# Optimization experiments

Measured on AMD Instinct MI355X. Metric: run time of the kernel, lower is better.

Reference implementation:

```python
import jax, jax.numpy as jnp
import numpy as np

N_NODES = 89250


def _sage_conv(x, src, dst, w_l, w_r, b):
    # mean aggregation of neighbor messages x[src] at destination nodes
    msg = x[src]                                                # [E, C]
    agg = jax.ops.segment_sum(msg, dst, num_segments=N_NODES)   # [N, C]
    cnt = jax.ops.segment_sum(jnp.ones((src.shape[0],), x.dtype), dst,
                              num_segments=N_NODES)             # [N]
    mean = agg / jnp.clip(cnt, 1.0, None)[:, None]
    # PyG SAGEConv: lin_l(aggregated) + lin_r(x) + bias
    return mean @ w_l.T + x @ w_r.T + b


def setup_inputs() -> dict:
    key = jax.random.key(0)
    ks = jax.random.split(key, 9)
    N, E, F_IN = N_NODES, 899756, 500

    def glorot(k, shape):
        fan_in = shape[1]
        return jax.random.normal(k, shape, jnp.float32) / jnp.sqrt(jnp.float32(fan_in))

    x = jax.random.normal(ks[0], (N, F_IN), jnp.float32)
    edge_index = jax.random.randint(ks[1], (2, E), 0, N, jnp.int64 if jax.config.jax_enable_x64 else jnp.int32)
    return {
        "x": x,
        "edge_index": edge_index,
        "w_l1": glorot(ks[2], (512, F_IN)),
        "w_r1": glorot(ks[3], (512, F_IN)),
        "b1": jnp.zeros((512,), jnp.float32),
        "w_l2": glorot(ks[4], (256, 512)),
        "w_r2": glorot(ks[5], (256, 512)),
        "b2": jnp.zeros((256,), jnp.float32),
        "w_l3": glorot(ks[6], (7, 256)),
        "w_r3": glorot(ks[7], (7, 256)),
        "b3": jnp.zeros((7,), jnp.float32),
    }


def reference(x, edge_index, w_l1, w_r1, b1, w_l2, w_r2, b2, w_l3, w_r3, b3):
    src, dst = edge_index[0], edge_index[1]
    # eval mode: dropout is identity
    h = jax.nn.relu(_sage_conv(x, src, dst, w_l1, w_r1, b1))
    h = jax.nn.relu(_sage_conv(h, src, dst, w_l2, w_r2, b2))
    return _sage_conv(h, src, dst, w_l3, w_r3, b3)
```

## Files before the change

### kernel.cpp

```cpp
#include <hip/hip_runtime.h>
#include <cstdint>
#include <cstddef>

#define N_NODES 89250
#define M_PAD   89344
#define F0 500
#define F1 512
#define F2 256
#define F3 7
#define KP 512

typedef __attribute__((ext_vector_type(8))) short bf16x8;
typedef __attribute__((ext_vector_type(4))) float f32x4;

static inline int cdiv_i(int a, int b) { return (a + b - 1) / b; }

__device__ __forceinline__ unsigned short f2b(float f) {
  unsigned int u = __float_as_uint(f);
  u = (u + 0x7FFFu + ((u >> 16) & 1u)) >> 16;
  return (unsigned short)u;
}
__device__ __forceinline__ float b2f(unsigned short h) {
  return __uint_as_float(((unsigned int)h) << 16);
}

__global__ void degree_kernel(const int* __restrict__ dst, int* __restrict__ cnt, int E) {
  int stride = gridDim.x * blockDim.x;
  for (int i = blockIdx.x * blockDim.x + threadIdx.x; i < E; i += stride)
    atomicAdd(&cnt[dst[i]], 1);
}

__global__ __launch_bounds__(1024) void scan_partial(const int* __restrict__ cnt,
                                                     int* __restrict__ row_ptr,
                                                     int* __restrict__ bsum, int n) {
  __shared__ int sm[1024];
  const int i = blockIdx.x * 1024 + threadIdx.x;
  const int v = (i < n) ? cnt[i] : 0;
  sm[threadIdx.x] = v;
  __syncthreads();
  for (int off = 1; off < 1024; off <<= 1) {
    int t = (threadIdx.x >= off) ? sm[threadIdx.x - off] : 0;
    __syncthreads();
    sm[threadIdx.x] += t;
    __syncthreads();
  }
  if (i < n) row_ptr[i] = sm[threadIdx.x] - v;
  if (threadIdx.x == 1023) bsum[blockIdx.x] = sm[1023];
}

__global__ __launch_bounds__(1024) void scan_bsums(int* __restrict__ bsum, int nb) {
  __shared__ int sm[1024];
  const int v = (threadIdx.x < nb) ? bsum[threadIdx.x] : 0;
  sm[threadIdx.x] = v;
  __syncthreads();
  for (int off = 1; off < 1024; off <<= 1) {
    int t = (threadIdx.x >= off) ? sm[threadIdx.x - off] : 0;
    __syncthreads();
    sm[threadIdx.x] += t;
    __syncthreads();
  }
  if (threadIdx.x < nb) bsum[threadIdx.x] = sm[threadIdx.x] - v;
}

__global__ __launch_bounds__(1024) void scan_add(int* __restrict__ row_ptr,
                                                 const int* __restrict__ bsum,
                                                 int* __restrict__ cursor,
                                                 int n, int total) {
  const int i = blockIdx.x * 1024 + threadIdx.x;
  if (i < n) {
    const int v = row_ptr[i] + bsum[i >> 10];
    row_ptr[i] = v;
    cursor[i] = v;
  }
  if (i == 0) row_ptr[n] = total;
}

__global__ void fill_kernel(const int* __restrict__ src, const int* __restrict__ dst,
                            int* __restrict__ cursor, int* __restrict__ csr_src, int E) {
  int stride = gridDim.x * blockDim.x;
  for (int i = blockIdx.x * blockDim.x + threadIdx.x; i < E; i += stride) {
    const int p = atomicAdd(&cursor[dst[i]], 1);
    csr_src[p] = src[i];
  }
}

#define XBLK (M_PAD * 64 / 256)
__global__ __launch_bounds__(256) void prep_kernel(
    const float* __restrict__ x,
    const float* __restrict__ wl1, const float* __restrict__ wr1,
    const float* __restrict__ wl2, const float* __restrict__ wr2,
    const float* __restrict__ wl3, const float* __restrict__ wr3,
    unsigned short* __restrict__ xb,
    unsigned short* __restrict__ wl1b, unsigned short* __restrict__ wr1b,
    unsigned short* __restrict__ w2b, unsigned short* __restrict__ w3b)
{
  if (blockIdx.x < XBLK) {
    const int idx = blockIdx.x * 256 + threadIdx.x;
    const int node = idx >> 6;
    const int c8 = (idx & 63) * 8;
    unsigned short r[8];
#pragma unroll
    for (int j = 0; j < 8; ++j) {
      const int c = c8 + j;
      float v = 0.0f;
      if (node < N_NODES && c < F0) v = x[(size_t)node * F0 + c];
      r[j] = f2b(v);
    }
    *reinterpret_cast<uint4*>(xb + (size_t)node * KP + c8) = *reinterpret_cast<const uint4*>(r);
    return;
  }
  int idx = (blockIdx.x - XBLK) * 256 + threadIdx.x;
  const int S1 = F1 * KP;
  if (idx < S1) {
    const int j = idx >> 9, k = idx & 511;
    const bool in = (k < F0);
    wl1b[idx] = in ? f2b(wl1[(size_t)j * F0 + k]) : (unsigned short)0;
    wr1b[idx] = in ? f2b(wr1[(size_t)j * F0 + k]) : (unsigned short)0;
    return;
  }
  idx -= S1;
  const int S2 = F2 * KP;
  if (idx < S2) {
    w2b[idx] = f2b(wl2[idx]);
    w2b[S2 + idx] = f2b(wr2[idx]);
    return;
  }
  idx -= S2;
  if (idx < 16 * 256) {
    const int j = idx >> 8, k = idx & 255;
    float v = 0.0f;
    if (j < 7) v = wl3[(size_t)j * F2 + k];
    else if (j >= 8 && j < 15) v = wr3[(size_t)(j - 8) * F2 + k];
    w3b[idx] = f2b(v);
  }
}

__global__ __launch_bounds__(256) void gather_mean_bf512(
    const unsigned short* __restrict__ xb, const int* __restrict__ row_ptr,
    const int* __restrict__ csr_src, unsigned short* __restrict__ aggb)
{
  const int node = blockIdx.x * 4 + (threadIdx.x >> 6);
  const int t = threadIdx.x & 63;
  if (node >= M_PAD) return;
  if (node >= N_NODES) {
    *reinterpret_cast<uint4*>(aggb + (size_t)node * 512 + t * 8) = make_uint4(0, 0, 0, 0);
    return;
  }
  const int beg = row_ptr[node];
  const int end = row_ptr[node + 1];
  float acc[8] = {0.f, 0.f, 0.f, 0.f, 0.f, 0.f, 0.f, 0.f};
  for (int j = beg; j < end; j += 8) {
    uint4 v[8];
    float m[8];
#pragma unroll
    for (int u = 0; u < 8; ++u) {
      const int e = min(j + u, end - 1);
      m[u] = (j + u < end) ? 1.0f : 0.0f;
      v[u] = *reinterpret_cast<const uint4*>(xb + (size_t)csr_src[e] * 512 + t * 8);
    }
#pragma unroll
    for (int u = 0; u < 8; ++u) {
      const unsigned int w[4] = {v[u].x, v[u].y, v[u].z, v[u].w};
#pragma unroll
      for (int q = 0; q < 4; ++q) {
        acc[2 * q]     = fmaf(m[u], b2f((unsigned short)(w[q] & 0xFFFF)), acc[2 * q]);
        acc[2 * q + 1] = fmaf(m[u], b2f((unsigned short)(w[q] >> 16)),    acc[2 * q + 1]);
      }
    }
  }
  const int deg = end - beg;
  const float inv = 1.0f / (float)(deg > 1 ? deg : 1);
  unsigned short r[8];
#pragma unroll
  for (int q = 0; q < 8; ++q) r[q] = f2b(acc[q] * inv);
  *reinterpret_cast<uint4*>(aggb + (size_t)node * 512 + t * 8) = *reinterpret_cast<const uint4*>(r);
}

__global__ __launch_bounds__(256) void gemm_mfma(
    const unsigned short* __restrict__ A1, const unsigned short* __restrict__ A2,
    const unsigned short* __restrict__ B1, const unsigned short* __restrict__ B2,
    const float* __restrict__ bias, unsigned short* __restrict__ Cout,
    int J, int niter, int fuse, int relu)
{
  __shared__ __align__(16) unsigned short Alds[128 * 64];
  __shared__ __align__(16) unsigned short Blds[128 * 64];
  const int tid = threadIdx.x;
  const int lane = tid & 63;
  const int wid = tid >> 6;

  const int nwg = gridDim.x * gridDim.y;
  int wg = blockIdx.y * gridDim.x + blockIdx.x;
  const int cpx = nwg >> 3;
  wg = (wg & 7) * cpx + (wg >> 3);
  const int brow = (wg / gridDim.y) * 128;
  const int bcol = (wg % gridDim.y) * 128;

  const int wr = wid >> 1;
  const int wc = wid & 1;

  f32x4 acc[4][4];
#pragma unroll
  for (int m = 0; m < 4; ++m)
#pragma unroll
    for (int n = 0; n < 4; ++n) acc[m][n] = (f32x4){0.f, 0.f, 0.f, 0.f};

  const int srow = lane >> 3;
  const int schunk = (lane & 7) ^ srow;
  const int fr = lane & 15;
  const int fk = lane >> 4;

  for (int it = 0; it < niter; ++it) {
    const unsigned short* __restrict__ A = (it < 8) ? A1 : A2;
    const unsigned short* __restrict__ B = (it < 8) ? B1 : B2;
    const int k0 = (it & 7) * 64;
    __syncthreads();
#pragma unroll
    for (int i = 0; i < 4; ++i) {
      const int rbase = i * 32 + wid * 8;
      const int row = rbase + srow;
      __builtin_amdgcn_global_load_lds(
          (const __attribute__((address_space(1))) unsigned int*)(A + (size_t)(brow + row) * KP + k0 + schunk * 8),
          (__attribute__((address_space(3))) unsigned int*)(&Alds[rbase * 64]),
          16, 0, 0);
      __builtin_amdgcn_global_load_lds(
          (const __attribute__((address_space(1))) unsigned int*)(B + (size_t)(bcol + row) * KP + k0 + schunk * 8),
          (__attribute__((address_space(3))) unsigned int*)(&Blds[rbase * 64]),
          16, 0, 0);
    }
    __syncthreads();
#pragma unroll
    for (int ks = 0; ks < 2; ++ks) {
      bf16x8 a[4], b[4];
#pragma unroll
      for (int m = 0; m < 4; ++m) {
        const int row = wr * 64 + m * 16 + fr;
        a[m] = *reinterpret_cast<const bf16x8*>(&Alds[row * 64 + (((ks * 4 + fk) ^ (row & 7)) * 8)]);
      }
#pragma unroll
      for (int n = 0; n < 4; ++n) {
        const int row = wc * 64 + n * 16 + fr;
        b[n] = *reinterpret_cast<const bf16x8*>(&Blds[row * 64 + (((ks * 4 + fk) ^ (row & 7)) * 8)]);
      }
#pragma unroll
      for (int m = 0; m < 4; ++m)
#pragma unroll
        for (int n = 0; n < 4; ++n)
          acc[m][n] = __builtin_amdgcn_mfma_f32_16x16x32_bf16(a[m], b[n], acc[m][n], 0, 0, 0);
    }
  }

  const int crow0 = brow + wr * 64 + (lane >> 4) * 4;
  const int ccol0 = bcol + wc * 64 + (lane & 15);
#pragma unroll
  for (int n = 0; n < 4; ++n) {
    const int col = ccol0 + n * 16;
    const float bv = fuse ? bias[col] : 0.0f;
#pragma unroll
    for (int m = 0; m < 4; ++m) {
#pragma unroll
      for (int i = 0; i < 4; ++i) {
        const int row = crow0 + m * 16 + i;
        float v = acc[m][n][i] + bv;
        if (relu) v = fmaxf(v, 0.0f);
        Cout[(size_t)row * J + col] = f2b(v);
      }
    }
  }
}

__global__ __launch_bounds__(256) void combine2p3_kernel(
    const unsigned short* __restrict__ y, const int* __restrict__ row_ptr,
    const int* __restrict__ csr_src, const float* __restrict__ bias,
    const unsigned short* __restrict__ w3b, unsigned short* __restrict__ y3)
{
  __shared__ unsigned short w3s[16 * 256];
  {
    const int t0 = threadIdx.x * 16;
    *reinterpret_cast<uint4*>(&w3s[t0])     = *reinterpret_cast<const uint4*>(&w3b[t0]);
    *reinterpret_cast<uint4*>(&w3s[t0 + 8]) = *reinterpret_cast<const uint4*>(&w3b[t0 + 8]);
  }
  __syncthreads();

  const int node = blockIdx.x * 8 + (threadIdx.x >> 5);
  const int t = threadIdx.x & 31;
  if (node >= N_NODES) return;
  const int beg = row_ptr[node];
  const int end = row_ptr[node + 1];
  float acc[8] = {0.f, 0.f, 0.f, 0.f, 0.f, 0.f, 0.f, 0.f};
  for (int j = beg; j < end; j += 8) {
    uint4 v[8];
    float m[8];
#pragma unroll
    for (int u = 0; u < 8; ++u) {
      const int e = min(j + u, end - 1);
      m[u] = (j + u < end) ? 1.0f : 0.0f;
      v[u] = *reinterpret_cast<const uint4*>(y + (size_t)csr_src[e] * 512 + t * 8);
    }
#pragma unroll
    for (int u = 0; u < 8; ++u) {
      const unsigned int w[4] = {v[u].x, v[u].y, v[u].z, v[u].w};
#pragma unroll
      for (int q = 0; q < 4; ++q) {
        acc[2 * q]     = fmaf(m[u], b2f((unsigned short)(w[q] & 0xFFFF)), acc[2 * q]);
        acc[2 * q + 1] = fmaf(m[u], b2f((unsigned short)(w[q] >> 16)),    acc[2 * q + 1]);
      }
    }
  }
  const int deg = end - beg;
  const float inv = 1.0f / (float)(deg > 1 ? deg : 1);
  const uint4 rv = *reinterpret_cast<const uint4*>(y + (size_t)node * 512 + 256 + t * 8);
  const unsigned int ru[4] = {rv.x, rv.y, rv.z, rv.w};
  float c[8];
#pragma unroll
  for (int q = 0; q < 4; ++q) {
    const float y0 = b2f((unsigned short)(ru[q] & 0xFFFF));
    const float y1 = b2f((unsigned short)(ru[q] >> 16));
    c[2 * q]     = fmaxf(acc[2 * q] * inv + y0 + bias[t * 8 + 2 * q], 0.0f);
    c[2 * q + 1] = fmaxf(acc[2 * q + 1] * inv + y1 + bias[t * 8 + 2 * q + 1], 0.0f);
  }
#pragma unroll
  for (int jj = 0; jj < 14; ++jj) {
    const int row = jj + (jj >= 7 ? 1 : 0);
    const uint4 wv = *reinterpret_cast<const uint4*>(&w3s[row * 256 + t * 8]);
    const unsigned int wu[4] = {wv.x, wv.y, wv.z, wv.w};
    float s = 0.0f;
#pragma unroll
    for (int q = 0; q < 4; ++q) {
      s = fmaf(c[2 * q],     b2f((unsigned short)(wu[q] & 0xFFFF)), s);
      s = fmaf(c[2 * q + 1], b2f((unsigned short)(wu[q] >> 16)),    s);
    }
#pragma unroll
    for (int m = 1; m < 32; m <<= 1) s += __shfl_xor(s, m, 64);
    if (t == 0) y3[(size_t)node * 16 + row] = f2b(s);
  }
}

__global__ __launch_bounds__(256) void combine3_kernel(
    const unsigned short* __restrict__ y3, const int* __restrict__ row_ptr,
    const int* __restrict__ csr_src, const float* __restrict__ b3,
    float* __restrict__ out, int N)
{
  const int node = blockIdx.x * 4 + (threadIdx.x >> 6);
  const int lane = threadIdx.x & 63;
  if (node >= N) return;
  const int beg = row_ptr[node];
  const int end = row_ptr[node + 1];
  float acc[7] = {0.f, 0.f, 0.f, 0.f, 0.f, 0.f, 0.f};
  for (int j = beg + lane; j < end; j += 64) {
    const int s = csr_src[j];
    const uint4 v = *reinterpret_cast<const uint4*>(y3 + (size_t)s * 16);
    const unsigned int u[4] = {v.x, v.y, v.z, v.w};
#pragma unroll
    for (int q = 0; q < 7; ++q) {
      const unsigned short hw = (unsigned short)((u[q >> 1] >> ((q & 1) * 16)) & 0xFFFF);
      acc[q] += b2f(hw);
    }
  }
#pragma unroll
  for (int q = 0; q < 7; ++q)
#pragma unroll
    for (int m = 1; m < 64; m <<= 1)
      acc[q] += __shfl_xor(acc[q], m, 64);
  if (lane == 0) {
    const int deg = end - beg;
    const float inv = 1.0f / (float)(deg > 1 ? deg : 1);
    const uint4 rv = *reinterpret_cast<const uint4*>(y3 + (size_t)node * 16 + 8);
    const unsigned int ru[4] = {rv.x, rv.y, rv.z, rv.w};
#pragma unroll
    for (int q = 0; q < 7; ++q) {
      const float self = b2f((unsigned short)((ru[q >> 1] >> ((q & 1) * 16)) & 0xFFFF));
      out[(size_t)node * F3 + q] = acc[q] * inv + self + b3[q];
    }
  }
}

extern "C" void kernel_launch(void* const* d_in, const int* in_sizes, int n_in,
                              void* d_out, int out_size, void* d_ws, size_t ws_size,
                              hipStream_t stream) {
  const float* x    = (const float*)d_in[0];
  const int*   ei   = (const int*)d_in[1];
  const float* w_l1 = (const float*)d_in[2];
  const float* w_r1 = (const float*)d_in[3];
  const float* b1   = (const float*)d_in[4];
  const float* w_l2 = (const float*)d_in[5];
  const float* w_r2 = (const float*)d_in[6];
  const float* b2   = (const float*)d_in[7];
  const float* w_l3 = (const float*)d_in[8];
  const float* w_r3 = (const float*)d_in[9];
  const float* b3   = (const float*)d_in[10];
  float* out = (float*)d_out;

  const int E = in_sizes[1] / 2;
  const int* src = ei;
  const int* dst = ei + E;

  char* p = (char*)d_ws;
  int* row_ptr = (int*)p;           p += (size_t)(N_NODES + 1) * 4;
  int* cnt     = (int*)p;           p += (size_t)N_NODES * 4;
  int* bsum    = (int*)p;           p += 1024 * 4;
  int* csr_src = (int*)p;           p += (size_t)E * 4;
  p = (char*)(((uintptr_t)p + 255) & ~(uintptr_t)255);
  unsigned short* xb   = (unsigned short*)p;  p += (size_t)M_PAD * KP * 2;
  unsigned short* aggb = (unsigned short*)p;  p += (size_t)M_PAD * KP * 2;
  unsigned short* h1b  = (unsigned short*)p;  p += (size_t)M_PAD * KP * 2;
  unsigned short* wl1b = (unsigned short*)p;  p += (size_t)F1 * KP * 2;
  unsigned short* wr1b = (unsigned short*)p;  p += (size_t)F1 * KP * 2;
  unsigned short* w2b  = (unsigned short*)p;  p += (size_t)F1 * KP * 2;
  unsigned short* w3b  = (unsigned short*)p;  p += (size_t)16 * F2 * 2;

  unsigned short* y2  = xb;
  unsigned short* y3  = h1b;

  const int nb = cdiv_i(N_NODES, 1024);

  hipMemsetAsync(cnt, 0, (size_t)N_NODES * sizeof(int), stream);
  degree_kernel<<<cdiv_i(E, 256), 256, 0, stream>>>(dst, cnt, E);
  scan_partial<<<nb, 1024, 0, stream>>>(cnt, row_ptr, bsum, N_NODES);
  scan_bsums<<<1, 1024, 0, stream>>>(bsum, nb);
  scan_add<<<nb, 1024, 0, stream>>>(row_ptr, bsum, cnt, N_NODES, E);
  fill_kernel<<<cdiv_i(E, 256), 256, 0, stream>>>(src, dst, cnt, csr_src, E);

  {
    const int wblocks = cdiv_i(F1 * KP + F2 * KP + 16 * F2, 256);
    prep_kernel<<<XBLK + wblocks, 256, 0, stream>>>(
        x, w_l1, w_r1, w_l2, w_r2, w_l3, w_r3, xb, wl1b, wr1b, w2b, w3b);
  }

  gather_mean_bf512<<<cdiv_i(M_PAD, 4), 256, 0, stream>>>(xb, row_ptr, csr_src, aggb);
  {
    dim3 g(M_PAD / 128, F1 / 128);
    gemm_mfma<<<g, 256, 0, stream>>>(aggb, xb, wl1b, wr1b, b1, h1b, F1, 16, 1, 1);
  }

  {
    dim3 g(M_PAD / 128, 512 / 128);
    gemm_mfma<<<g, 256, 0, stream>>>(h1b, h1b, w2b, w2b, (const float*)nullptr, y2, 512, 8, 0, 0);
  }
  combine2p3_kernel<<<cdiv_i(N_NODES, 8), 256, 0, stream>>>(y2, row_ptr, csr_src, b2, w3b, y3);

  combine3_kernel<<<cdiv_i(N_NODES, 4), 256, 0, stream>>>(y3, row_ptr, csr_src, b3, out, N_NODES);
}
```

Before: 637.5 us.

## Use 256x256 double-buffered MFMA GEMM tiles with 8 waves and prefetch

The bf16 MFMA GEMM moves from 128x128 tiles with 4 waves to 256x256 tiles with 8 waves per block. The LDS buffers for A and B are now double-buffered so the next K-slice loads overlap the current MFMA work, with one barrier per iteration instead of two. Wave priority is raised around the MFMA bursts and the XCD block remapping now handles grid sizes that do not divide by 8. The larger tiles raise operand reuse and cut global traffic, but use 128KB of LDS and more accumulator registers, which limits occupancy to about one block per CU and leaves fewer blocks in the grid.

```diff
diff --git a/kernel.cpp b/kernel.cpp
--- a/kernel.cpp
+++ b/kernel.cpp
@@ -176,87 +176,106 @@
   *reinterpret_cast<uint4*>(aggb + (size_t)node * 512 + t * 8) = *reinterpret_cast<const uint4*>(r);
 }
 
-__global__ __launch_bounds__(256) void gemm_mfma(
+__global__ __launch_bounds__(512) void gemm_mfma256(
     const unsigned short* __restrict__ A1, const unsigned short* __restrict__ A2,
     const unsigned short* __restrict__ B1, const unsigned short* __restrict__ B2,
     const float* __restrict__ bias, unsigned short* __restrict__ Cout,
-    int J, int niter, int fuse, int relu)
+    int J, int nt, int fuse, int relu)
 {
-  __shared__ __align__(16) unsigned short Alds[128 * 64];
-  __shared__ __align__(16) unsigned short Blds[128 * 64];
+  __shared__ __align__(16) unsigned short Alds[2][256 * 64];
+  __shared__ __align__(16) unsigned short Blds[2][256 * 64];
   const int tid = threadIdx.x;
   const int lane = tid & 63;
-  const int wid = tid >> 6;
-
-  const int nwg = gridDim.x * gridDim.y;
-  int wg = blockIdx.y * gridDim.x + blockIdx.x;
-  const int cpx = nwg >> 3;
-  wg = (wg & 7) * cpx + (wg >> 3);
-  const int brow = (wg / gridDim.y) * 128;
-  const int bcol = (wg % gridDim.y) * 128;
-
-  const int wr = wid >> 1;
-  const int wc = wid & 1;
-
-  f32x4 acc[4][4];
-#pragma unroll
-  for (int m = 0; m < 4; ++m)
+  const int w = tid >> 6;
+  const int wm = w >> 2;
+  const int wn = w & 3;
+
+  int wg = blockIdx.x;
+  {
+    const int nwg = gridDim.x;
+    const int q = nwg >> 3, r = nwg & 7;
+    const int xcd = wg & 7, o = wg >> 3;
+    wg = (xcd < r ? xcd * (q + 1) : r * (q + 1) + (xcd - r) * q) + o;
+  }
+  const int ncol = J >> 8;
+  const int brow = (wg / ncol) * 256;
+  const int bcol = (wg % ncol) * 256;
+
+  f32x4 acc[8][4];
+#pragma unroll
+  for (int m = 0; m < 8; ++m)
 #pragma unroll
     for (int n = 0; n < 4; ++n) acc[m][n] = (f32x4){0.f, 0.f, 0.f, 0.f};
 
+  const int fr = lane & 15;
+  const int fk = lane >> 4;
   const int srow = lane >> 3;
   const int schunk = (lane & 7) ^ srow;
-  const int fr = lane & 15;
-  const int fk = lane >> 4;
-
-  for (int it = 0; it < niter; ++it) {
-    const unsigned short* __restrict__ A = (it < 8) ? A1 : A2;
-    const unsigned short* __restrict__ B = (it < 8) ? B1 : B2;
-    const int k0 = (it & 7) * 64;
-    __syncthreads();
-#pragma unroll
-    for (int i = 0; i < 4; ++i) {
-      const int rbase = i * 32 + wid * 8;
+
+  auto STAGE_H = [&](int t, int which) {
+    const int h = which >> 1;
+    const int k0 = (t & 7) * 64;
+    const int buf = t & 1;
+    const unsigned short* __restrict__ src;
+    unsigned short* ldsb;
+    if (which & 1) { src = (t < 8) ? B1 : B2; ldsb = Blds[buf]; }
+    else           { src = (t < 8) ? A1 : A2; ldsb = Alds[buf]; }
+    const int gbase = (which & 1) ? bcol : brow;
+#pragma unroll
+    for (int i = 0; i < 2; ++i) {
+      const int rbase = h * 128 + i * 64 + w * 8;
       const int row = rbase + srow;
       __builtin_amdgcn_global_load_lds(
-          (const __attribute__((address_space(1))) unsigned int*)(A + (size_t)(brow + row) * KP + k0 + schunk * 8),
-          (__attribute__((address_space(3))) unsigned int*)(&Alds[rbase * 64]),
+          (const __attribute__((address_space(1))) unsigned int*)(src + (size_t)(gbase + row) * KP + k0 + schunk * 8),
+          (__attribute__((address_space(3))) unsigned int*)(ldsb + rbase * 64),
           16, 0, 0);
-      __builtin_amdgcn_global_load_lds(
-          (const __attribute__((address_space(1))) unsigned int*)(B + (size_t)(bcol + row) * KP + k0 + schunk * 8),
-          (__attribute__((address_space(3))) unsigned int*)(&Blds[rbase * 64]),
-          16, 0, 0);
-    }
-    __syncthreads();
-#pragma unroll
-    for (int ks = 0; ks < 2; ++ks) {
-      bf16x8 a[4], b[4];
+    }
+  };
+
+#pragma unroll
+  for (int p = 0; p < 4; ++p) STAGE_H(0, p);
+
+  for (int t = 0; t < nt; ++t) {
+    asm volatile("s_waitcnt vmcnt(0)" ::: "memory");
+    asm volatile("s_barrier" ::: "memory");
+    const int buf = t & 1;
+    bf16x8 bb[4];
+#pragma unroll
+    for (int p = 0; p < 4; ++p) {
+      if (t + 1 < nt) STAGE_H(t + 1, p);
+      const int mh = p & 1;
+      const int ks = p >> 1;
+      bf16x8 a[4];
 #pragma unroll
       for (int m = 0; m < 4; ++m) {
-        const int row = wr * 64 + m * 16 + fr;
-        a[m] = *reinterpret_cast<const bf16x8*>(&Alds[row * 64 + (((ks * 4 + fk) ^ (row & 7)) * 8)]);
+        const int row = wm * 128 + (mh * 4 + m) * 16 + fr;
+        a[m] = *reinterpret_cast<const bf16x8*>(&Alds[buf][row * 64 + (((ks * 4 + fk) ^ (row & 7)) * 8)]);
       }
-#pragma unroll
-      for (int n = 0; n < 4; ++n) {
-        const int row = wc * 64 + n * 16 + fr;
-        b[n] = *reinterpret_cast<const bf16x8*>(&Blds[row * 64 + (((ks * 4 + fk) ^ (row & 7)) * 8)]);
+      if (mh == 0) {
+#pragma unroll
+        for (int n = 0; n < 4; ++n) {
+          const int row = wn * 64 + n * 16 + fr;
+          bb[n] = *reinterpret_cast<const bf16x8*>(&Blds[buf][row * 64 + (((ks * 4 + fk) ^ (row & 7)) * 8)]);
+        }
       }
+      __builtin_amdgcn_s_setprio(1);
 #pragma unroll
       for (int m = 0; m < 4; ++m)
 #pragma unroll
         for (int n = 0; n < 4; ++n)
-          acc[m][n] = __builtin_amdgcn_mfma_f32_16x16x32_bf16(a[m], b[n], acc[m][n], 0, 0, 0);
-    }
-  }
-
-  const int crow0 = brow + wr * 64 + (lane >> 4) * 4;
-  const int ccol0 = bcol + wc * 64 + (lane & 15);
+          acc[mh * 4 + m][n] = __builtin_amdgcn_mfma_f32_16x16x32_bf16(a[m], bb[n], acc[mh * 4 + m][n], 0, 0, 0);
+      __builtin_amdgcn_s_setprio(0);
+    }
+  }
+
+  const int crow0 = brow + wm * 128 + (lane >> 4) * 4;
+  const int ccol0 = bcol + wn * 64 + fr;
 #pragma unroll
   for (int n = 0; n < 4; ++n) {
     const int col = ccol0 + n * 16;
     const float bv = fuse ? bias[col] : 0.0f;
 #pragma unroll
-    for (int m = 0; m < 4; ++m) {
+    for (int m = 0; m < 8; ++m) {
 #pragma unroll
       for (int i = 0; i < 4; ++i) {
         const int row = crow0 + m * 16 + i;
@@ -427,15 +446,11 @@
   }
 
   gather_mean_bf512<<<cdiv_i(M_PAD, 4), 256, 0, stream>>>(xb, row_ptr, csr_src, aggb);
-  {
-    dim3 g(M_PAD / 128, F1 / 128);
-    gemm_mfma<<<g, 256, 0, stream>>>(aggb, xb, wl1b, wr1b, b1, h1b, F1, 16, 1, 1);
-  }
-
-  {
-    dim3 g(M_PAD / 128, 512 / 128);
-    gemm_mfma<<<g, 256, 0, stream>>>(h1b, h1b, w2b, w2b, (const float*)nullptr, y2, 512, 8, 0, 0);
-  }
+  gemm_mfma256<<<(M_PAD / 256) * (F1 / 256), 512, 0, stream>>>(
+      aggb, xb, wl1b, wr1b, b1, h1b, F1, 16, 1, 1);
+
+  gemm_mfma256<<<(M_PAD / 256) * (512 / 256), 512, 0, stream>>>(
+      h1b, h1b, w2b, w2b, (const float*)nullptr, y2, 512, 8, 0, 0);
   combine2p3_kernel<<<cdiv_i(N_NODES, 8), 256, 0, stream>>>(y2, row_ptr, csr_src, b2, w3b, y3);
 
   combine3_kernel<<<cdiv_i(N_NODES, 4), 256, 0, stream>>>(y3, row_ptr, csr_src, b3, out, N_NODES);
```

Result: slower. 671.0 us (+5.3%).
